# Kernel optimization log

Hardware: AMD Instinct MI355X
Metric: run time of the kernel (lower is better)

## Reference

```python
import jax, jax.numpy as jnp
import numpy as np

N, E = 50000, 1600000
D_IN, D_HID, D_OUT = 256, 256, 128  # 2*output_dim = 256, output_dim = 128


def glorot(key, shape):
    fan_in, fan_out = shape
    limit = np.sqrt(6.0 / (fan_in + fan_out)).astype(np.float32)
    return jax.random.uniform(key, shape, jnp.float32, -limit, limit)


def setup_inputs() -> dict:
    key = jax.random.key(0)
    k0, k1, k2, k3 = jax.random.split(key, 4)
    x = jax.random.normal(k0, (N, D_IN), jnp.float32)
    edge_index = jax.random.randint(k1, (2, E), 0, N, jnp.int32)
    W1 = glorot(k2, (D_IN, D_HID))
    b1 = jnp.zeros((D_HID,), jnp.float32)
    W2 = glorot(k3, (D_HID, D_OUT))
    b2 = jnp.zeros((D_OUT,), jnp.float32)
    return {"x": x, "edge_index": edge_index, "W1": W1, "b1": b1, "W2": W2, "b2": b2}


def gcn_propagate(x, src, dst, num_nodes):
    """One hop of D^-1/2 (A + I) D^-1/2 @ x (PyG gcn_norm with self-loops)."""
    loops = jnp.arange(num_nodes, dtype=src.dtype)
    src_sl = jnp.concatenate([src, loops])  # [E + N]
    dst_sl = jnp.concatenate([dst, loops])
    ones = jnp.ones(src_sl.shape, x.dtype)
    deg = jax.ops.segment_sum(ones, dst_sl, num_segments=num_nodes)  # >= 1 (self-loop)
    dinv = jax.lax.rsqrt(jnp.maximum(deg, 1e-12))
    norm = dinv[src_sl] * dinv[dst_sl]  # [E + N]
    msgs = x[src_sl] * norm[:, None]    # gather + scale, [E+N, D]
    return jax.ops.segment_sum(msgs, dst_sl, num_segments=num_nodes)


def reference(x, edge_index, W1, b1, W2, b2):
    src, dst = edge_index[0], edge_index[1]
    n = x.shape[0]
    # SGConv(K=1): propagate then linear. conv1 + ReLU
    h = jax.nn.relu(gcn_propagate(x, src, dst, n) @ W1 + b1)
    # conv2 (GAE branch)
    return gcn_propagate(h, src, dst, n) @ W2 + b2
```

## Files before the change

### kernel.cpp

```cpp
#include <hip/hip_runtime.h>

typedef short s16x8 __attribute__((ext_vector_type(8)));
typedef float f32x4 __attribute__((ext_vector_type(4)));
typedef float f32x2 __attribute__((ext_vector_type(2)));

#define TILE 2048

__device__ __forceinline__ unsigned int brne(float f) {
    unsigned int u = __float_as_uint(f);
    return (u + 0x7FFFu + ((u >> 16) & 1u)) >> 16;
}
__device__ __forceinline__ float blo(unsigned int u) { return __uint_as_float(u << 16); }
__device__ __forceinline__ float bhi(unsigned int u) { return __uint_as_float(u & 0xFFFF0000u); }

__device__ __forceinline__ unsigned int pk_bf16(float lo, float hi) {
    unsigned int r;
    asm("v_cvt_pk_bf16_f32 %0, %1, %2" : "=v"(r) : "v"(lo), "v"(hi));
    return r;
}

__device__ __forceinline__ void pkfma(f32x2& a, const f32x2 x, const f32x2 w) {
    asm("v_pk_fma_f32 %0, %1, %2, %0" : "+v"(a) : "v"(x), "v"(w));
}

__device__ __forceinline__ void acc8p(f32x2* a, const uint4 u, const f32x2 w2) {
    pkfma(a[0], (f32x2){blo(u.x), bhi(u.x)}, w2);
    pkfma(a[1], (f32x2){blo(u.y), bhi(u.y)}, w2);
    pkfma(a[2], (f32x2){blo(u.z), bhi(u.z)}, w2);
    pkfma(a[3], (f32x2){blo(u.w), bhi(u.w)}, w2);
}

__device__ __forceinline__ void acc16p(f32x2* a, const uint4 u, const f32x2 w2) {
    pkfma(a[0], __builtin_amdgcn_cvt_pk_f32_fp8((int)u.x, false), w2);
    pkfma(a[1], __builtin_amdgcn_cvt_pk_f32_fp8((int)u.x, true),  w2);
    pkfma(a[2], __builtin_amdgcn_cvt_pk_f32_fp8((int)u.y, false), w2);
    pkfma(a[3], __builtin_amdgcn_cvt_pk_f32_fp8((int)u.y, true),  w2);
    pkfma(a[4], __builtin_amdgcn_cvt_pk_f32_fp8((int)u.z, false), w2);
    pkfma(a[5], __builtin_amdgcn_cvt_pk_f32_fp8((int)u.z, true),  w2);
    pkfma(a[6], __builtin_amdgcn_cvt_pk_f32_fp8((int)u.w, false), w2);
    pkfma(a[7], __builtin_amdgcn_cvt_pk_f32_fp8((int)u.w, true),  w2);
}


__global__ void k_scatter_deg_tw(const int* __restrict__ src, const int* __restrict__ dst,
                                 int* __restrict__ bcnt, int* __restrict__ deg,
                                 uint2* __restrict__ eb, int e, int cap, int nbt,
                                 const float* __restrict__ W1, const float* __restrict__ W2,
                                 unsigned short* __restrict__ W1t, unsigned short* __restrict__ W2t) {
    const int tid = threadIdx.x;
    if ((int)blockIdx.x >= nbt) {
        const int t = ((int)blockIdx.x - nbt) * 256 + tid;
        if (t < 65536) {
            const int k = t >> 8, nn = t & 255;
            W1t[nn * 256 + k] = (unsigned short)brne(W1[t]);
        } else {
            const int u = t - 65536;
            const int k = u >> 7, nn = u & 127;
            W2t[nn * 256 + k] = (unsigned short)brne(W2[u]);
        }
        return;
    }
    __shared__ int h[256], hbase[256], h2[256];
    h[tid] = 0; h2[tid] = 0;
    __syncthreads();
    const int base = blockIdx.x * TILE + tid;
    int s[8], d[8];
    bool val[8];
#pragma unroll
    for (int k = 0; k < 8; k++) {
        const int i = base + k * 256;
        val[k] = i < e;
        if (val[k]) {
            s[k] = src[i]; d[k] = dst[i];
            atomicAdd(&h[d[k] >> 8], 1);
            atomicAdd(&deg[d[k]], 1);
        }
    }
    __syncthreads();
    if (h[tid]) hbase[tid] = atomicAdd(&bcnt[tid], h[tid]);
    __syncthreads();
#pragma unroll
    for (int k = 0; k < 8; k++) {
        if (val[k]) {
            const int b = d[k] >> 8;
            const int off = atomicAdd(&h2[b], 1);
            eb[(size_t)b * cap + hbase[b] + off] = make_uint2((unsigned)s[k], (unsigned)d[k]);
        }
    }
}

template <bool PREW>
__global__ void k_scan1(const int* __restrict__ deg, int* __restrict__ rowptr,
                        int* __restrict__ part, float* __restrict__ dinv,
                        void* __restrict__ esv, int n, int e) {
    __shared__ int sh[256];
    const int tid = threadIdx.x, b = blockIdx.x;
    const int node = b * 256 + tid;
    const int v = (node < n) ? deg[node] : 0;
    if (node < n) dinv[node] = rsqrtf((float)(v + 1));
    int x = v;
    sh[tid] = x;
    __syncthreads();
    for (int off = 1; off < 256; off <<= 1) {
        const int t = (tid >= off) ? sh[tid - off] : 0;
        __syncthreads();
        if (tid >= off) { x += t; sh[tid] = x; }
        __syncthreads();
    }
    if (node <= n) rowptr[node] = x - v;
    if (tid == 255) part[b] = x;
    if (PREW && b == 0 && tid < 64) ((int2*)esv)[e + tid] = make_int2(0, 0);
}

template <bool PREW>
__global__ void k_place3(const uint2* __restrict__ eb, const int* __restrict__ bcnt,
                         int* __restrict__ rowptr, const int* __restrict__ part,
                         const float* __restrict__ dinv, void* __restrict__ esv,
                         int n, int nb, int cap) {
    __shared__ int sh[256], rp[256], offs[256];
    __shared__ float sdv[256];
    const int tid = threadIdx.x, b = blockIdx.x;
    int x = (tid < nb) ? part[tid] : 0;
    sh[tid] = x;
    __syncthreads();
    for (int off = 1; off < 256; off <<= 1) {
        const int t = (tid >= off) ? sh[tid - off] : 0;
        __syncthreads();
        if (tid >= off) { x += t; sh[tid] = x; }
        __syncthreads();
    }
    const int prefix = (b > 0) ? sh[b - 1] : 0;
    const int node = b * 256 + tid;
    int rg = 0;
    if (node <= n) {
        rg = rowptr[node] + prefix;
        rowptr[node] = rg;
    }
    rp[tid] = rg;
    offs[tid] = 0;
    if (PREW) sdv[tid] = (node < n) ? dinv[node] : 0.f;
    __syncthreads();
    const int cnt = bcnt[b];
    const size_t bb = (size_t)b * cap;
    if (PREW) {
        int2* es2 = (int2*)esv;
        for (int i = tid; i < cnt; i += 256) {
            const uint2 ed = eb[bb + i];
            const int sI = (int)ed.x, d = (int)ed.y & 255;
            const float w = dinv[sI] * sdv[d];
            const int local = atomicAdd(&offs[d], 1);
            es2[rp[d] + local] = make_int2(sI, __float_as_int(w));
        }
    } else {
        int* es1 = (int*)esv;
        for (int i = tid; i < cnt; i += 256) {
            const uint2 ed = eb[bb + i];
            const int d = (int)ed.y & 255;
            const int local = atomicAdd(&offs[d], 1);
            es1[rp[d] + local] = (int)ed.x;
        }
    }
}

#define LP 40
template <bool AF32, bool FP8OUT>
__global__ __launch_bounds__(256) void k_gemm(const void* __restrict__ Av,
                                              const unsigned short* __restrict__ Bt,
                                              void* __restrict__ Cout,
                                              int M, int Nc) {
    __shared__ unsigned short As[2][128 * LP];
    __shared__ unsigned short Bs[2][128 * LP];

    const int tid = threadIdx.x;
    const int wave = tid >> 6, lane = tid & 63;
    const int wm = (wave >> 1) * 64, wn = (wave & 1) * 64;
    const int l15 = lane & 15, quad = lane >> 4;
    const int mBase = blockIdx.x * 128, nBase = blockIdx.y * 128;

    f32x4 acc[4][4];
#pragma unroll
    for (int i = 0; i < 4; i++)
#pragma unroll
        for (int j = 0; j < 4; j++) acc[i][j] = (f32x4){0.f, 0.f, 0.f, 0.f};

    const int r0 = tid >> 2, kc0 = tid & 3;
    int am0 = mBase + r0;      if (am0 >= M) am0 = M - 1;
    int am1 = mBase + r0 + 64; if (am1 >= M) am1 = M - 1;

    const uint4* Ap0; const uint4* Ap1; const float4* Af0; const float4* Af1;
    if (AF32) {
        Af0 = (const float4*)Av + (size_t)am0 * 64 + kc0 * 2;
        Af1 = (const float4*)Av + (size_t)am1 * 64 + kc0 * 2;
    } else {
        Ap0 = (const uint4*)Av + (size_t)am0 * 32 + kc0;
        Ap1 = (const uint4*)Av + (size_t)am1 * 32 + kc0;
    }
    const uint4* Bp0 = (const uint4*)Bt + (size_t)(nBase + r0) * 32 + kc0;
    const uint4* Bp1 = (const uint4*)Bt + (size_t)(nBase + r0 + 64) * 32 + kc0;

    uint4 a0, a1, b0, b1;
    auto LOAD = [&](int kt) {
        if (AF32) {
            const float4 l0 = Af0[kt * 8], h0 = Af0[kt * 8 + 1];
            const float4 l1 = Af1[kt * 8], h1 = Af1[kt * 8 + 1];
            a0.x = pk_bf16(l0.x, l0.y); a0.y = pk_bf16(l0.z, l0.w);
            a0.z = pk_bf16(h0.x, h0.y); a0.w = pk_bf16(h0.z, h0.w);
            a1.x = pk_bf16(l1.x, l1.y); a1.y = pk_bf16(l1.z, l1.w);
            a1.z = pk_bf16(h1.x, h1.y); a1.w = pk_bf16(h1.z, h1.w);
        } else {
            a0 = Ap0[kt * 4];
            a1 = Ap1[kt * 4];
        }
        b0 = Bp0[kt * 4];
        b1 = Bp1[kt * 4];
    };
    auto STORE = [&](int buf) {
        *(uint4*)&As[buf][r0 * LP + kc0 * 8] = a0;
        *(uint4*)&As[buf][(r0 + 64) * LP + kc0 * 8] = a1;
        *(uint4*)&Bs[buf][r0 * LP + kc0 * 8] = b0;
        *(uint4*)&Bs[buf][(r0 + 64) * LP + kc0 * 8] = b1;
    };

    LOAD(0);
    STORE(0);
    __syncthreads();
    for (int kt = 0; kt < 8; ++kt) {
        const int cur = kt & 1;
        if (kt < 7) LOAD(kt + 1);
        s16x8 af[4], bf[4];
#pragma unroll
        for (int i = 0; i < 4; i++)
            af[i] = *(const s16x8*)&As[cur][(wm + i * 16 + l15) * LP + quad * 8];
#pragma unroll
        for (int j = 0; j < 4; j++)
            bf[j] = *(const s16x8*)&Bs[cur][(wn + j * 16 + l15) * LP + quad * 8];
        if (kt < 7) STORE(cur ^ 1);
#pragma unroll
        for (int i = 0; i < 4; i++)
#pragma unroll
            for (int j = 0; j < 4; j++)
                acc[i][j] = __builtin_amdgcn_mfma_f32_16x16x32_bf16(af[i], bf[j], acc[i][j], 0, 0, 0);
        __syncthreads();
    }

#pragma unroll
    for (int i = 0; i < 4; i++) {
        const int rowb = mBase + wm + i * 16 + quad * 4;
#pragma unroll
        for (int j = 0; j < 4; j++) {
            const int col = nBase + wn + j * 16 + l15;
#pragma unroll
            for (int r = 0; r < 4; r += 2) {
                if (FP8OUT) {
                    const unsigned int pk = __builtin_amdgcn_cvt_pk_fp8_f32(
                        acc[i][j][r], acc[i][j][r + 1], 0, false);
                    if (rowb + r < M)
                        ((unsigned char*)Cout)[(size_t)(rowb + r) * Nc + col] =
                            (unsigned char)pk;
                    if (rowb + r + 1 < M)
                        ((unsigned char*)Cout)[(size_t)(rowb + r + 1) * Nc + col] =
                            (unsigned char)(pk >> 8);
                } else {
                    const unsigned int pk = pk_bf16(acc[i][j][r], acc[i][j][r + 1]);
                    if (rowb + r < M)
                        ((unsigned short*)Cout)[(size_t)(rowb + r) * Nc + col] =
                            (unsigned short)pk;
                    if (rowb + r + 1 < M)
                        ((unsigned short*)Cout)[(size_t)(rowb + r + 1) * Nc + col] =
                            (unsigned short)(pk >> 16);
                }
            }
        }
    }
}


template <bool PREW>
__global__ void k_prop256f8(const uint4* __restrict__ X4,
                            const int* __restrict__ rowptr,
                            const void* __restrict__ esv,
                            const float* __restrict__ dinv,
                            const float* __restrict__ bias,
                            uint4* __restrict__ Y4, int n) {
    const int wid = (int)((blockIdx.x * blockDim.x + threadIdx.x) >> 6);
    const int lane = threadIdx.x & 63;
    const int quad = lane >> 4, l16 = lane & 15;
    if (wid >= n) return;
    const float dd = dinv[wid];
    const int2* es2 = (const int2*)esv;
    const int*  es1 = (const int*)esv;
    f32x2 a[8];
#pragma unroll
    for (int k = 0; k < 8; k++) a[k] = (f32x2){0.f, 0.f};

    const int beg = rowptr[wid], end = rowptr[wid + 1];
    int j = beg + quad;

    auto EDGE = [&](int jj, int& s, float& w) {
        const bool v = jj < end;
        const int idx = v ? jj : beg;
        if (PREW) {
            const int2 p = es2[idx];
            s = p.x;
            w = v ? __int_as_float(p.y) : 0.f;
        } else {
            s = es1[v ? jj : 0];
            w = v ? dinv[s] * dd : 0.f;
        }
    };

    int s0, s1, s2, s3;
    float w0, w1, w2, w3;
    EDGE(j, s0, w0); EDGE(j + 4, s1, w1); EDGE(j + 8, s2, w2); EDGE(j + 12, s3, w3);

    if (quad == 0) {
        const uint4 v = X4[(size_t)wid * 16 + l16];
        acc16p(a, v, (f32x2){dd * dd, dd * dd});
    }

    while (j + 12 < end) {
        const uint4 u0 = X4[(size_t)s0 * 16 + l16];
        const uint4 u1 = X4[(size_t)s1 * 16 + l16];
        const uint4 u2 = X4[(size_t)s2 * 16 + l16];
        const uint4 u3 = X4[(size_t)s3 * 16 + l16];
        j += 16;
        int t0, t1, t2, t3;
        float x0, x1, x2, x3;
        EDGE(j, t0, x0); EDGE(j + 4, t1, x1); EDGE(j + 8, t2, x2); EDGE(j + 12, t3, x3);
        acc16p(a, u0, (f32x2){w0, w0});
        acc16p(a, u1, (f32x2){w1, w1});
        acc16p(a, u2, (f32x2){w2, w2});
        acc16p(a, u3, (f32x2){w3, w3});
        s0 = t0; s1 = t1; s2 = t2; s3 = t3;
        w0 = x0; w1 = x1; w2 = x2; w3 = x3;
    }
    {
        const uint4 u0 = X4[(size_t)s0 * 16 + l16];
        const uint4 u1 = X4[(size_t)s1 * 16 + l16];
        const uint4 u2 = X4[(size_t)s2 * 16 + l16];
        acc16p(a, u0, (f32x2){w0, w0});
        acc16p(a, u1, (f32x2){w1, w1});
        acc16p(a, u2, (f32x2){w2, w2});
    }
#pragma unroll
    for (int k = 0; k < 8; k++) {
        a[k][0] += __shfl_xor(a[k][0], 16);
        a[k][1] += __shfl_xor(a[k][1], 16);
        a[k][0] += __shfl_xor(a[k][0], 32);
        a[k][1] += __shfl_xor(a[k][1], 32);
    }
    if (quad == 0) {
        const float4* bp = (const float4*)bias + l16 * 4;
#pragma unroll
        for (int q = 0; q < 4; q++) {
            const float4 b = bp[q];
            a[2 * q][0]     = fmaxf(a[2 * q][0] + b.x, 0.f);
            a[2 * q][1]     = fmaxf(a[2 * q][1] + b.y, 0.f);
            a[2 * q + 1][0] = fmaxf(a[2 * q + 1][0] + b.z, 0.f);
            a[2 * q + 1][1] = fmaxf(a[2 * q + 1][1] + b.w, 0.f);
        }
        uint4 p0, p1;
        p0.x = pk_bf16(a[0][0], a[0][1]);
        p0.y = pk_bf16(a[1][0], a[1][1]);
        p0.z = pk_bf16(a[2][0], a[2][1]);
        p0.w = pk_bf16(a[3][0], a[3][1]);
        p1.x = pk_bf16(a[4][0], a[4][1]);
        p1.y = pk_bf16(a[5][0], a[5][1]);
        p1.z = pk_bf16(a[6][0], a[6][1]);
        p1.w = pk_bf16(a[7][0], a[7][1]);
        Y4[(size_t)wid * 32 + l16 * 2] = p0;
        Y4[(size_t)wid * 32 + l16 * 2 + 1] = p1;
    }
}

template <bool PREW>
__global__ void k_prop128b(const uint4* __restrict__ X4,
                           const int* __restrict__ rowptr,
                           const void* __restrict__ esv,
                           const float* __restrict__ dinv,
                           const float* __restrict__ bias,
                           float* __restrict__ Yout, int n) {
    const int wid = (int)((blockIdx.x * blockDim.x + threadIdx.x) >> 6);
    const int lane = threadIdx.x & 63;
    const int quad = lane >> 4, l16 = lane & 15;
    if (wid >= n) return;
    const float dd = dinv[wid];
    const int2* es2 = (const int2*)esv;
    const int*  es1 = (const int*)esv;
    f32x2 a[4];
#pragma unroll
    for (int k = 0; k < 4; k++) a[k] = (f32x2){0.f, 0.f};

    const int beg = rowptr[wid], end = rowptr[wid + 1];
    int j = beg + quad;

    auto EDGE = [&](int jj, int& s, float& w) {
        const bool v = jj < end;
        const int idx = v ? jj : beg;
        if (PREW) {
            const int2 p = es2[idx];
            s = p.x;
            w = v ? __int_as_float(p.y) : 0.f;
        } else {
            s = es1[v ? jj : 0];
            w = v ? dinv[s] * dd : 0.f;
        }
    };

    int s0, s1, s2, s3;
    float w0, w1, w2, w3;
    EDGE(j, s0, w0); EDGE(j + 4, s1, w1); EDGE(j + 8, s2, w2); EDGE(j + 12, s3, w3);

    if (quad == 0) {
        const uint4 v = X4[(size_t)wid * 16 + l16];
        acc8p(a, v, (f32x2){dd * dd, dd * dd});
    }

    while (j + 12 < end) {
        const uint4 u0 = X4[(size_t)s0 * 16 + l16];
        const uint4 u1 = X4[(size_t)s1 * 16 + l16];
        const uint4 u2 = X4[(size_t)s2 * 16 + l16];
        const uint4 u3 = X4[(size_t)s3 * 16 + l16];
        j += 16;
        int t0, t1, t2, t3;
        float x0, x1, x2, x3;
        EDGE(j, t0, x0); EDGE(j + 4, t1, x1); EDGE(j + 8, t2, x2); EDGE(j + 12, t3, x3);
        acc8p(a, u0, (f32x2){w0, w0});
        acc8p(a, u1, (f32x2){w1, w1});
        acc8p(a, u2, (f32x2){w2, w2});
        acc8p(a, u3, (f32x2){w3, w3});
        s0 = t0; s1 = t1; s2 = t2; s3 = t3;
        w0 = x0; w1 = x1; w2 = x2; w3 = x3;
    }
    {
        const uint4 u0 = X4[(size_t)s0 * 16 + l16];
        const uint4 u1 = X4[(size_t)s1 * 16 + l16];
        const uint4 u2 = X4[(size_t)s2 * 16 + l16];
        acc8p(a, u0, (f32x2){w0, w0});
        acc8p(a, u1, (f32x2){w1, w1});
        acc8p(a, u2, (f32x2){w2, w2});
    }
#pragma unroll
    for (int k = 0; k < 4; k++) {
        a[k][0] += __shfl_xor(a[k][0], 16);
        a[k][1] += __shfl_xor(a[k][1], 16);
        a[k][0] += __shfl_xor(a[k][0], 32);
        a[k][1] += __shfl_xor(a[k][1], 32);
    }
    if (quad == 0) {
        const float4 b0 = ((const float4*)bias)[l16 * 2];
        const float4 b1 = ((const float4*)bias)[l16 * 2 + 1];
        float4* op = (float4*)Yout + (size_t)wid * 32 + l16 * 2;
        op[0] = make_float4(a[0][0] + b0.x, a[0][1] + b0.y, a[1][0] + b0.z, a[1][1] + b0.w);
        op[1] = make_float4(a[2][0] + b1.x, a[2][1] + b1.y, a[3][0] + b1.z, a[3][1] + b1.w);
    }
}

extern "C" void kernel_launch(void* const* d_in, const int* in_sizes, int n_in,
                              void* d_out, int out_size, void* d_ws, size_t ws_size,
                              hipStream_t stream) {
    const float* x  = (const float*)d_in[0];
    const int*   ei = (const int*)d_in[1];
    const float* W1 = (const float*)d_in[2];
    const float* b1 = (const float*)d_in[3];
    const float* W2 = (const float*)d_in[4];
    const float* b2 = (const float*)d_in[5];
    float* out = (float*)d_out;

    const int n = in_sizes[0] / 256;
    const int e = in_sizes[1] / 2;
    const int* src = ei;
    const int* dst = ei + e;
    const int nb = (n + 255) >> 8;

    int cap = (((e / nb) * 3 / 2) + 1023) & ~1023;
    if (cap < 2048) cap = 2048;

    auto al = [](size_t v) { return (v + 511) & ~(size_t)511; };
    const size_t fixed = al(sizeof(float) * n) + al(sizeof(int) * (n + 1)) +
                         al(1024) + al(4ull * (256 + n)) +
                         al(2ull * 256 * 256) + al(2ull * 128 * 256) +
                         al((size_t)n * 256) + al(2ull * n * 256) + al(2ull * n * 128);
    const bool prew = (fixed + al(8ull * ((size_t)e + 64))) <= ws_size;

    char* wsp = (char*)d_ws;
    size_t off = 0;
    auto alloc = [&](size_t bytes) -> char* {
        char* p = wsp + off;
        off += (bytes + 511) & ~(size_t)511;
        return p;
    };
    float* dinv    = (float*)alloc(sizeof(float) * n);
    int*   rowptr  = (int*)alloc(sizeof(int) * (n + 1));
    int*   part    = (int*)alloc(1024);
    int*   bcd     = (int*)alloc(4ull * (256 + n));
    int*   bcnt    = bcd;
    int*   deg     = bcd + 256;
    void*  es      = (void*)alloc(prew ? 8ull * ((size_t)e + 64) : 4ull * (size_t)e);
    unsigned short* W1t = (unsigned short*)alloc(2ull * 256 * 256);
    unsigned short* W2t = (unsigned short*)alloc(2ull * 128 * 256);
    unsigned char*  T1  = (unsigned char*)alloc((size_t)n * 256);
    unsigned short* H   = (unsigned short*)alloc(2ull * n * 256);
    unsigned short* T2  = (unsigned short*)alloc(2ull * n * 128);
    uint2* eb = (uint2*)H;
    {
        const size_t hbytes = 2ull * n * 256;
        if ((size_t)nb * cap * 8ull > hbytes) cap = (int)(hbytes / ((size_t)nb * 8ull));
    }

    const int nb_t = (e + TILE - 1) / TILE;
    const int tw_b = (65536 + 32768) / 256;

    (void)hipMemsetAsync(bcd, 0, 4ull * (256 + n), stream);
    k_scatter_deg_tw<<<nb_t + tw_b, 256, 0, stream>>>(src, dst, bcnt, deg, eb, e, cap,
                                                      nb_t, W1, W2, W1t, W2t);
    if (prew) {
        k_scan1<true><<<nb, 256, 0, stream>>>(deg, rowptr, part, dinv, es, n, e);
        k_place3<true><<<nb, 256, 0, stream>>>(eb, bcnt, rowptr, part, dinv, es, n, nb, cap);
    } else {
        k_scan1<false><<<nb, 256, 0, stream>>>(deg, rowptr, part, dinv, es, n, e);
        k_place3<false><<<nb, 256, 0, stream>>>(eb, bcnt, rowptr, part, dinv, es, n, nb, cap);
    }

    dim3 g1((n + 127) / 128, 2);
    k_gemm<true, true><<<g1, 256, 0, stream>>>(x, W1t, T1, n, 256);
    if (prew)
        k_prop256f8<true><<<(n + 3) / 4, 256, 0, stream>>>((const uint4*)T1, rowptr, es,
                                                           dinv, b1, (uint4*)H, n);
    else
        k_prop256f8<false><<<(n + 3) / 4, 256, 0, stream>>>((const uint4*)T1, rowptr, es,
                                                            dinv, b1, (uint4*)H, n);

    dim3 g2((n + 127) / 128, 1);
    k_gemm<false, false><<<g2, 256, 0, stream>>>(H, W2t, T2, n, 128);
    if (prew)
        k_prop128b<true><<<(n + 3) / 4, 256, 0, stream>>>((const uint4*)T2, rowptr, es,
                                                          dinv, b2, out, n);
    else
        k_prop128b<false><<<(n + 3) / 4, 256, 0, stream>>>((const uint4*)T2, rowptr, es,
                                                           dinv, b2, out, n);
}
```

Measured before the change: 355.5 us.

## Replace fixed-capacity bucket scatter with histogram-then-compact two-pass bucketing

```diff
diff --git a/kernel.cpp b/kernel.cpp
--- a/kernel.cpp
+++ b/kernel.cpp
@@ -5,6 +5,7 @@
 typedef float f32x2 __attribute__((ext_vector_type(2)));
 
 #define TILE 2048
+#define TILE2 8192
 
 __device__ __forceinline__ unsigned int brne(float f) {
     unsigned int u = __float_as_uint(f);
@@ -42,11 +43,10 @@
 }
 
 
-__global__ void k_scatter_deg_tw(const int* __restrict__ src, const int* __restrict__ dst,
-                                 int* __restrict__ bcnt, int* __restrict__ deg,
-                                 uint2* __restrict__ eb, int e, int cap, int nbt,
-                                 const float* __restrict__ W1, const float* __restrict__ W2,
-                                 unsigned short* __restrict__ W1t, unsigned short* __restrict__ W2t) {
+__global__ void k_bhist_deg_tw(const int* __restrict__ dst, int* __restrict__ bcnt,
+                               int* __restrict__ deg, int e, int nb, int nbt,
+                               const float* __restrict__ W1, const float* __restrict__ W2,
+                               unsigned short* __restrict__ W1t, unsigned short* __restrict__ W2t) {
     const int tid = threadIdx.x;
     if ((int)blockIdx.x >= nbt) {
         const int t = ((int)blockIdx.x - nbt) * 256 + tid;
@@ -60,32 +60,53 @@
         }
         return;
     }
-    __shared__ int h[256], hbase[256], h2[256];
-    h[tid] = 0; h2[tid] = 0;
+    __shared__ int h[256];
+    h[tid] = 0;
     __syncthreads();
     const int base = blockIdx.x * TILE + tid;
-    int s[8], d[8];
-    bool val[8];
 #pragma unroll
     for (int k = 0; k < 8; k++) {
         const int i = base + k * 256;
-        val[k] = i < e;
-        if (val[k]) {
-            s[k] = src[i]; d[k] = dst[i];
-            atomicAdd(&h[d[k] >> 8], 1);
-            atomicAdd(&deg[d[k]], 1);
-        }
-    }
-    __syncthreads();
-    if (h[tid]) hbase[tid] = atomicAdd(&bcnt[tid], h[tid]);
-    __syncthreads();
-#pragma unroll
-    for (int k = 0; k < 8; k++) {
-        if (val[k]) {
-            const int b = d[k] >> 8;
-            const int off = atomicAdd(&h2[b], 1);
-            eb[(size_t)b * cap + hbase[b] + off] = make_uint2((unsigned)s[k], (unsigned)d[k]);
-        }
+        if (i < e) {
+            const int d = dst[i];
+            atomicAdd(&h[d >> 8], 1);
+            atomicAdd(&deg[d], 1);
+        }
+    }
+    __syncthreads();
+    if (tid < nb && h[tid]) atomicAdd(&bcnt[tid], h[tid]);
+}
+
+__global__ void k_bscatter8(const int* __restrict__ src, const int* __restrict__ dst,
+                            const int* __restrict__ bcnt, int* __restrict__ bcur,
+                            uint2* __restrict__ eb, int e, int nb) {
+    __shared__ int sh[256], h[256], base2[256], h2[256];
+    const int tid = threadIdx.x;
+    const int v = (tid < nb) ? bcnt[tid] : 0;
+    int x = v;
+    sh[tid] = x;
+    __syncthreads();
+    for (int off = 1; off < 256; off <<= 1) {
+        const int t = (tid >= off) ? sh[tid - off] : 0;
+        __syncthreads();
+        if (tid >= off) { x += t; sh[tid] = x; }
+        __syncthreads();
+    }
+    const int sbase = x - v;
+    h[tid] = 0; h2[tid] = 0;
+    __syncthreads();
+    const int beg = blockIdx.x * TILE2;
+    const int fin = min(beg + TILE2, e);
+    for (int i = beg + tid; i < fin; i += 256)
+        atomicAdd(&h[dst[i] >> 8], 1);
+    __syncthreads();
+    if (h[tid]) base2[tid] = sbase + atomicAdd(&bcur[tid], h[tid]);
+    __syncthreads();
+    for (int i = beg + tid; i < fin; i += 256) {
+        const int s = src[i], d = dst[i];
+        const int b = d >> 8;
+        const int off = atomicAdd(&h2[b], 1);
+        eb[base2[b] + off] = make_uint2((unsigned)s, (unsigned)d);
     }
 }
 
@@ -116,17 +137,30 @@
 __global__ void k_place3(const uint2* __restrict__ eb, const int* __restrict__ bcnt,
                          int* __restrict__ rowptr, const int* __restrict__ part,
                          const float* __restrict__ dinv, void* __restrict__ esv,
-                         int n, int nb, int cap) {
+                         int n, int nb) {
     __shared__ int sh[256], rp[256], offs[256];
     __shared__ float sdv[256];
     const int tid = threadIdx.x, b = blockIdx.x;
-    int x = (tid < nb) ? part[tid] : 0;
+    const int cv = (tid < nb) ? bcnt[tid] : 0;
+    int x = cv;
     sh[tid] = x;
     __syncthreads();
     for (int off = 1; off < 256; off <<= 1) {
         const int t = (tid >= off) ? sh[tid - off] : 0;
         __syncthreads();
         if (tid >= off) { x += t; sh[tid] = x; }
+        __syncthreads();
+    }
+    const int ebBase = (b > 0) ? sh[b - 1] : 0;
+    const int cnt = bcnt[b];
+    __syncthreads();
+    int y = (tid < nb) ? part[tid] : 0;
+    sh[tid] = y;
+    __syncthreads();
+    for (int off = 1; off < 256; off <<= 1) {
+        const int t = (tid >= off) ? sh[tid - off] : 0;
+        __syncthreads();
+        if (tid >= off) { y += t; sh[tid] = y; }
         __syncthreads();
     }
     const int prefix = (b > 0) ? sh[b - 1] : 0;
@@ -140,12 +174,10 @@
     offs[tid] = 0;
     if (PREW) sdv[tid] = (node < n) ? dinv[node] : 0.f;
     __syncthreads();
-    const int cnt = bcnt[b];
-    const size_t bb = (size_t)b * cap;
     if (PREW) {
         int2* es2 = (int2*)esv;
         for (int i = tid; i < cnt; i += 256) {
-            const uint2 ed = eb[bb + i];
+            const uint2 ed = eb[ebBase + i];
             const int sI = (int)ed.x, d = (int)ed.y & 255;
             const float w = dinv[sI] * sdv[d];
             const int local = atomicAdd(&offs[d], 1);
@@ -154,7 +186,7 @@
     } else {
         int* es1 = (int*)esv;
         for (int i = tid; i < cnt; i += 256) {
-            const uint2 ed = eb[bb + i];
+            const uint2 ed = eb[ebBase + i];
             const int d = (int)ed.y & 255;
             const int local = atomicAdd(&offs[d], 1);
             es1[rp[d] + local] = (int)ed.x;
@@ -473,12 +505,9 @@
     const int* dst = ei + e;
     const int nb = (n + 255) >> 8;
 
-    int cap = (((e / nb) * 3 / 2) + 1023) & ~1023;
-    if (cap < 2048) cap = 2048;
-
     auto al = [](size_t v) { return (v + 511) & ~(size_t)511; };
     const size_t fixed = al(sizeof(float) * n) + al(sizeof(int) * (n + 1)) +
-                         al(1024) + al(4ull * (256 + n)) +
+                         al(1024) + al(4ull * (512 + n)) +
                          al(2ull * 256 * 256) + al(2ull * 128 * 256) +
                          al((size_t)n * 256) + al(2ull * n * 256) + al(2ull * n * 128);
     const bool prew = (fixed + al(8ull * ((size_t)e + 64))) <= ws_size;
@@ -493,9 +522,10 @@
     float* dinv    = (float*)alloc(sizeof(float) * n);
     int*   rowptr  = (int*)alloc(sizeof(int) * (n + 1));
     int*   part    = (int*)alloc(1024);
-    int*   bcd     = (int*)alloc(4ull * (256 + n));
+    int*   bcd     = (int*)alloc(4ull * (512 + n));
     int*   bcnt    = bcd;
-    int*   deg     = bcd + 256;
+    int*   bcur    = bcd + 256;
+    int*   deg     = bcd + 512;
     void*  es      = (void*)alloc(prew ? 8ull * ((size_t)e + 64) : 4ull * (size_t)e);
     unsigned short* W1t = (unsigned short*)alloc(2ull * 256 * 256);
     unsigned short* W2t = (unsigned short*)alloc(2ull * 128 * 256);
@@ -503,23 +533,21 @@
     unsigned short* H   = (unsigned short*)alloc(2ull * n * 256);
     unsigned short* T2  = (unsigned short*)alloc(2ull * n * 128);
     uint2* eb = (uint2*)H;
-    {
-        const size_t hbytes = 2ull * n * 256;
-        if ((size_t)nb * cap * 8ull > hbytes) cap = (int)(hbytes / ((size_t)nb * 8ull));
-    }
-
-    const int nb_t = (e + TILE - 1) / TILE;
-    const int tw_b = (65536 + 32768) / 256;
-
-    (void)hipMemsetAsync(bcd, 0, 4ull * (256 + n), stream);
-    k_scatter_deg_tw<<<nb_t + tw_b, 256, 0, stream>>>(src, dst, bcnt, deg, eb, e, cap,
-                                                      nb_t, W1, W2, W1t, W2t);
+
+    const int nb_t  = (e + TILE - 1) / TILE;
+    const int nb_t2 = (e + TILE2 - 1) / TILE2;
+    const int tw_b  = (65536 + 32768) / 256;
+
+    (void)hipMemsetAsync(bcd, 0, 4ull * (512 + n), stream);
+    k_bhist_deg_tw<<<nb_t + tw_b, 256, 0, stream>>>(dst, bcnt, deg, e, nb, nb_t,
+                                                    W1, W2, W1t, W2t);
+    k_bscatter8<<<nb_t2, 256, 0, stream>>>(src, dst, bcnt, bcur, eb, e, nb);
     if (prew) {
         k_scan1<true><<<nb, 256, 0, stream>>>(deg, rowptr, part, dinv, es, n, e);
-        k_place3<true><<<nb, 256, 0, stream>>>(eb, bcnt, rowptr, part, dinv, es, n, nb, cap);
+        k_place3<true><<<nb, 256, 0, stream>>>(eb, bcnt, rowptr, part, dinv, es, n, nb);
     } else {
         k_scan1<false><<<nb, 256, 0, stream>>>(deg, rowptr, part, dinv, es, n, e);
-        k_place3<false><<<nb, 256, 0, stream>>>(eb, bcnt, rowptr, part, dinv, es, n, nb, cap);
+        k_place3<false><<<nb, 256, 0, stream>>>(eb, bcnt, rowptr, part, dinv, es, n, nb);
     }
 
     dim3 g1((n + 127) / 128, 2);
```

After: 375.2 us. 1.06x slower.
